# Kernel optimization log

Hardware: AMD Instinct MI355X
Metric: run time of the kernel (lower is better)

Reference implementation:

```python
import jax, jax.numpy as jnp
import numpy as np

D = 1024          # d_model
H = 16            # num_attention_heads
HD = D // H       # head_dim
WIN = 512         # attention_window (total)
W = WIN // 2      # one-sided window
S = 4096          # seq_len
B = 2             # batch
NEG = jnp.finfo(jnp.float32).min


def setup_inputs() -> dict:
    key = jax.random.key(0)
    ks = jax.random.split(key, 9)
    sc = 0.02
    return {
        "query": jax.random.normal(ks[0], (S, B, D), dtype=jnp.float32),
        "Wq": jax.random.normal(ks[1], (D, D), dtype=jnp.float32) * sc,
        "bq": jnp.zeros((D,), dtype=jnp.float32),
        "Wk": jax.random.normal(ks[2], (D, D), dtype=jnp.float32) * sc,
        "bk": jnp.zeros((D,), dtype=jnp.float32),
        "Wv": jax.random.normal(ks[3], (D, D), dtype=jnp.float32) * sc,
        "bv": jnp.zeros((D,), dtype=jnp.float32),
        "Wo": jax.random.normal(ks[4], (D, D), dtype=jnp.float32) * sc,
        "bo": jnp.zeros((D,), dtype=jnp.float32),
    }


def _heads(x):  # [B,S,D] -> [B,H,S,HD]
    b, s, _ = x.shape
    return x.reshape(b, s, H, HD).transpose(0, 2, 1, 3)


def reference(query, Wq, bq, Wk, bk, Wv, bv, Wo, bo):
    s, b, d = query.shape
    x = query.transpose(1, 0, 2)                       # [B,S,D]
    q = _heads(x @ Wq + bq) / jnp.sqrt(jnp.float32(HD))  # [B,H,S,HD]
    k = _heads(x @ Wk + bk)
    v = _heads(x @ Wv + bv)

    nc = s // W                                        # number of chunks
    # pad keys/values with one window of zeros on each side of seq axis
    kp = jnp.pad(k, ((0, 0), (0, 0), (W, W), (0, 0)))  # [B,H,S+2W,HD]
    vp = jnp.pad(v, ((0, 0), (0, 0), (W, W), (0, 0)))
    idx = jnp.arange(nc)[:, None] * W + jnp.arange(3 * W)[None, :]  # [nc,3W]
    kc = kp[:, :, idx]                                 # [B,H,nc,3W,HD]
    vc = vp[:, :, idx]
    qc = q.reshape(b, H, nc, W, HD)                    # [B,H,nc,W,HD]

    scores = jnp.einsum("bhcrd,bhckd->bhcrk", qc, kc)  # [B,H,nc,W,3W]

    r = jnp.arange(W)[:, None]                         # query offset in chunk
    kk = jnp.arange(3 * W)[None, :]
    band = (kk >= r) & (kk <= r + 2 * W)               # |kpos-qpos| <= W
    kpos = jnp.arange(nc)[:, None, None] * W + kk[None] - W   # [nc,1,3W] global key pos
    mask = band[None] & (kpos >= 0) & (kpos < s)       # [nc,W,3W]

    scores = jnp.where(mask[None, None], scores, NEG)
    probs = jax.nn.softmax(scores, axis=-1)
    out = jnp.einsum("bhcrk,bhckd->bhcrd", probs, vc)  # [B,H,nc,W,HD]
    out = out.reshape(b, H, s, HD).transpose(0, 2, 1, 3).reshape(b, s, d)
    out = out.transpose(1, 0, 2)                       # [S,B,D]
    return out @ Wo + bo
```

## Files before the change

kernel.cpp:

```cpp
#include <hip/hip_runtime.h>
#include <hip/hip_bf16.h>

#define SEQ 4096
#define BATCH 2
#define DMODEL 1024
#define NH 16
#define HDIM 64
#define NEGM (-1.0e30f)
#define NT 16

typedef __attribute__((ext_vector_type(8))) short bf16x8;
typedef __attribute__((ext_vector_type(8))) unsigned short us8;
typedef __attribute__((ext_vector_type(4))) unsigned short us4;
typedef __attribute__((ext_vector_type(4))) float f32x4;

__device__ __forceinline__ unsigned short f2bf(float f) {
    union { float f; unsigned u; } v; v.f = f;
    unsigned u = v.u;
    return (unsigned short)((u + 0x7fffu + ((u >> 16) & 1u)) >> 16);
}

#define GL16(g, l)                                                              \
    __builtin_amdgcn_global_load_lds(                                           \
        (const __attribute__((address_space(1))) unsigned int*)(g),             \
        (__attribute__((address_space(3))) unsigned int*)(l), 16, 0, 0)

__global__ __launch_bounds__(256) void prep_all(const float* __restrict__ Wq,
                                                const float* __restrict__ Wk,
                                                const float* __restrict__ Wv,
                                                const float* __restrict__ Wo,
                                                const float* __restrict__ query,
                                                const float* __restrict__ bq,
                                                const float* __restrict__ bk,
                                                const float* __restrict__ bv,
                                                unsigned short* __restrict__ wcat,
                                                unsigned short* __restrict__ wot,
                                                unsigned short* __restrict__ xb,
                                                float* __restrict__ bcat) {
    __shared__ float tile[64][65];
    const int bid = blockIdx.x;
    const int tid = threadIdx.x;
    if (bid < 1024) {
        const int z = bid >> 8, by = (bid >> 4) & 15, bx = bid & 15;
        const float* W = (z == 0) ? Wq : (z == 1) ? Wk : (z == 2) ? Wv : Wo;
        unsigned short* Wt = (z == 3) ? wot : wcat + (size_t)z * 1024 * 1024;
        const float scale = (z == 0) ? 0.125f : 1.0f;
        const int n0 = bx * 64, k0 = by * 64;
        const int tx = tid & 63, ty = tid >> 6;
        for (int dy = ty; dy < 64; dy += 4)
            tile[dy][tx] = W[(size_t)(k0 + dy) * DMODEL + n0 + tx];
        __syncthreads();
        for (int dy = ty; dy < 64; dy += 4)
            Wt[(size_t)(n0 + dy) * DMODEL + k0 + tx] = f2bf(tile[tx][dy] * scale);
    } else if (bid < 9216) {
        int t = (bid - 1024) * 256 + tid;
        int d4 = (t & 255) * 4;
        int row = t >> 8;
        int b = row >> 12, s = row & (SEQ - 1);
        float4 v = *(const float4*)(query + ((size_t)s * BATCH + b) * DMODEL + d4);
        us4 o;
        o[0] = f2bf(v.x); o[1] = f2bf(v.y); o[2] = f2bf(v.z); o[3] = f2bf(v.w);
        *(us4*)(xb + (size_t)row * DMODEL + d4) = o;
    } else {
        int i = (bid - 9216) * 256 + tid;
        float v;
        if (i < 1024) v = bq[i] * 0.125f;
        else if (i < 2048) v = bk[i - 1024];
        else v = bv[i - 2048];
        bcat[i] = v;
    }
}

__device__ __forceinline__ void store_qkv(float v0, float v1, float v2, float v3,
                                          int row0, int col, float bval,
                                          unsigned short* __restrict__ qb,
                                          unsigned short* __restrict__ kb,
                                          unsigned short* __restrict__ vtb) {
    const int proj = col >> 10;
    const int ch = col & 1023;
    const int h = ch >> 6, hd = ch & 63;
    float vv[4] = {v0, v1, v2, v3};
    if (proj == 2) {
        const int b = row0 >> 12, s = row0 & (SEQ - 1);
        us4 o;
#pragma unroll
        for (int r = 0; r < 4; ++r) o[r] = f2bf(vv[r] + bval);
        *(us4*)(vtb + ((size_t)(b * NH + h) * HDIM + hd) * SEQ + s) = o;
    } else {
        unsigned short* dst = (proj == 0) ? qb : kb;
#pragma unroll
        for (int r = 0; r < 4; ++r) {
            const int row = row0 + r;
            const int b = row >> 12, s = row & (SEQ - 1);
            dst[((size_t)(b * NH + h) * SEQ + s) * HDIM + hd] = f2bf(vv[r] + bval);
        }
    }
}

__global__ __launch_bounds__(512) void gemm192(const unsigned short* __restrict__ A,
                                               const unsigned short* __restrict__ Bt,
                                               const float* __restrict__ bias,
                                               unsigned short* __restrict__ qb,
                                               unsigned short* __restrict__ kb,
                                               unsigned short* __restrict__ vtb) {
    __shared__ __align__(16) unsigned short lds[57344];
    const int tid = threadIdx.x;
    const int lane = tid & 63, wid = tid >> 6;
    const int lr = lane & 15, lg = lane >> 4;
    const int wm = wid >> 1, wn = wid & 1;
    const int cpx = (int)gridDim.x >> 3;
    const int orig = ((int)blockIdx.x & 7) * cpx + ((int)blockIdx.x >> 3);
    const int m0 = (orig >> 4) * 256;
    const int n0 = (orig & 15) * 192;

    const int srow = wid * 8 + (lane >> 3);
    const int scol = ((lane & 7) ^ (lane >> 3)) << 3;

    f32x4 acc[4][6];
#pragma unroll
    for (int m = 0; m < 4; ++m)
#pragma unroll
        for (int n = 0; n < 6; ++n) {
            f32x4 z = {0.f, 0.f, 0.f, 0.f};
            acc[m][n] = z;
        }

    const unsigned short* gA = A + (size_t)(m0 + srow) * DMODEL + scol;
    const unsigned short* gB = Bt + (size_t)(n0 + srow) * DMODEL + scol;

#define STAGE192(kt, bsel)                                                       \
    do {                                                                         \
        const unsigned short* ga_ = gA + (kt) * 64;                              \
        unsigned short* la_ = &lds[(bsel) * 28672 + wid * 512];                  \
        _Pragma("unroll")                                                        \
        for (int r_ = 0; r_ < 4; ++r_)                                           \
            GL16(ga_ + (size_t)r_ * 64 * DMODEL, la_ + r_ * 4096);               \
        const unsigned short* gb_ = gB + (kt) * 64;                              \
        unsigned short* lb_ = &lds[(bsel) * 28672 + 16384 + wid * 512];          \
        _Pragma("unroll")                                                        \
        for (int r_ = 0; r_ < 3; ++r_)                                           \
            GL16(gb_ + (size_t)r_ * 64 * DMODEL, lb_ + r_ * 4096);               \
    } while (0)

    STAGE192(0, 0);
    asm volatile("s_waitcnt vmcnt(0)" ::: "memory");
    __builtin_amdgcn_s_barrier();
    asm volatile("" ::: "memory");

    const int swz = (lr & 7) << 3;
    for (int t = 0; t < NT; ++t) {
        if (t + 1 < NT) STAGE192(t + 1, (t + 1) & 1);
        const unsigned short* Ab = &lds[(t & 1) * 28672];
        const unsigned short* Bb = Ab + 16384;
#pragma unroll
        for (int ks = 0; ks < 2; ++ks) {
            const int kc = (ks * 32 + lg * 8) ^ swz;
            bf16x8 af[4], bfr[6];
#pragma unroll
            for (int fm = 0; fm < 4; ++fm)
                af[fm] = *(const bf16x8*)&Ab[(wm * 64 + fm * 16 + lr) * 64 + kc];
#pragma unroll
            for (int fn = 0; fn < 6; ++fn)
                bfr[fn] = *(const bf16x8*)&Bb[(wn * 96 + fn * 16 + lr) * 64 + kc];
            __builtin_amdgcn_s_setprio(1);
#pragma unroll
            for (int fm = 0; fm < 4; ++fm)
#pragma unroll
                for (int fn = 0; fn < 6; ++fn)
                    acc[fm][fn] = __builtin_amdgcn_mfma_f32_16x16x32_bf16(af[fm], bfr[fn], acc[fm][fn], 0, 0, 0);
            __builtin_amdgcn_s_setprio(0);
        }
        __builtin_amdgcn_sched_barrier(0);
        asm volatile("s_waitcnt lgkmcnt(0)" ::: "memory");
        asm volatile("s_waitcnt vmcnt(0)" ::: "memory");
        __builtin_amdgcn_s_barrier();
        asm volatile("" ::: "memory");
    }
#undef STAGE192

#pragma unroll
    for (int fn = 0; fn < 6; ++fn) {
        const int col = n0 + wn * 96 + fn * 16 + lr;
        const float bval = bias[col];
#pragma unroll
        for (int fm = 0; fm < 4; ++fm) {
            const int row0 = m0 + wm * 64 + fm * 16 + lg * 4;
            store_qkv(acc[fm][fn][0], acc[fm][fn][1], acc[fm][fn][2], acc[fm][fn][3],
                      row0, col, bval, qb, kb, vtb);
        }
    }
}

__global__ __launch_bounds__(256, 4) void gemm128o(const unsigned short* __restrict__ A,
                                                   const unsigned short* __restrict__ Bt,
                                                   const float* __restrict__ bias,
                                                   float* __restrict__ out) {
    __shared__ __align__(16) unsigned short lds[16384];
    const int tid = threadIdx.x;
    const int lane = tid & 63, wid = tid >> 6;
    const int lr = lane & 15, lg = lane >> 4;
    const int wm = wid >> 1, wn = wid & 1;
    const int cpx = (int)gridDim.x >> 3;
    const int orig = ((int)blockIdx.x & 7) * cpx + ((int)blockIdx.x >> 3);
    const int m0 = (orig >> 3) * 128;
    const int n0 = (orig & 7) * 128;

    const int srow = wid * 8 + (lane >> 3);
    const int scol = ((lane & 7) ^ (lane >> 3)) << 3;

    f32x4 acc[4][4];
#pragma unroll
    for (int m = 0; m < 4; ++m)
#pragma unroll
        for (int n = 0; n < 4; ++n) {
            f32x4 z = {0.f, 0.f, 0.f, 0.f};
            acc[m][n] = z;
        }

    const unsigned short* gA = A + (size_t)(m0 + srow) * DMODEL + scol;
    const unsigned short* gB = Bt + (size_t)(n0 + srow) * DMODEL + scol;
    const int swz = (lr & 7) << 3;

    for (int t = 0; t < NT; ++t) {
        {
            const unsigned short* ga_ = gA + t * 64;
            unsigned short* la_ = &lds[wid * 512];
#pragma unroll
            for (int r_ = 0; r_ < 4; ++r_)
                GL16(ga_ + (size_t)r_ * 32 * DMODEL, la_ + r_ * 2048);
            const unsigned short* gb_ = gB + t * 64;
            unsigned short* lb_ = &lds[8192 + wid * 512];
#pragma unroll
            for (int r_ = 0; r_ < 4; ++r_)
                GL16(gb_ + (size_t)r_ * 32 * DMODEL, lb_ + r_ * 2048);
        }
        asm volatile("s_waitcnt vmcnt(0)" ::: "memory");
        __builtin_amdgcn_s_barrier();
        asm volatile("" ::: "memory");
#pragma unroll
        for (int ks = 0; ks < 2; ++ks) {
            const int kc = (ks * 32 + lg * 8) ^ swz;
            bf16x8 af[4], bfr[4];
#pragma unroll
            for (int fm = 0; fm < 4; ++fm)
                af[fm] = *(const bf16x8*)&lds[(wm * 64 + fm * 16 + lr) * 64 + kc];
#pragma unroll
            for (int fn = 0; fn < 4; ++fn)
                bfr[fn] = *(const bf16x8*)&lds[8192 + (wn * 64 + fn * 16 + lr) * 64 + kc];
            __builtin_amdgcn_s_setprio(1);
#pragma unroll
            for (int fm = 0; fm < 4; ++fm)
#pragma unroll
                for (int fn = 0; fn < 4; ++fn)
                    acc[fm][fn] = __builtin_amdgcn_mfma_f32_16x16x32_bf16(af[fm], bfr[fn], acc[fm][fn], 0, 0, 0);
            __builtin_amdgcn_s_setprio(0);
        }
        __builtin_amdgcn_sched_barrier(0);
        asm volatile("s_waitcnt lgkmcnt(0)" ::: "memory");
        __builtin_amdgcn_s_barrier();
        asm volatile("" ::: "memory");
    }

#pragma unroll
    for (int fn = 0; fn < 4; ++fn) {
        const int col = n0 + wn * 64 + fn * 16 + lr;
        const float bval = bias[col];
#pragma unroll
        for (int fm = 0; fm < 4; ++fm) {
            const int row0 = m0 + wm * 64 + fm * 16 + lg * 4;
#pragma unroll
            for (int r = 0; r < 4; ++r) {
                const int row = row0 + r;
                const int b = row >> 12, s = row & (SEQ - 1);
                out[((size_t)s * BATCH + b) * DMODEL + col] = acc[fm][fn][r] + bval;
            }
        }
    }
}

__global__ __launch_bounds__(512) void attn_kernel(const unsigned short* __restrict__ qb,
                                                   const unsigned short* __restrict__ kb,
                                                   const unsigned short* __restrict__ vtb,
                                                   unsigned short* __restrict__ ao) {
    __shared__ __align__(16) unsigned short Ks[64][72];
    __shared__ __align__(16) unsigned short Vs[64][72];
    __shared__ __align__(16) unsigned short Ps[8][16][72];
    const int tid = threadIdx.x;
    const int lane = tid & 63, wid = tid >> 6;
    const int lr = lane & 15, lg = lane >> 4;
    const int blk = ((int)blockIdx.x & 7) * 128 + ((int)blockIdx.x >> 3);
    const int qc = blk & 31, h = (blk >> 5) & 15, b = blk >> 9;
    const int q0 = qc * 128;
    const unsigned short* Qh = qb + (size_t)(b * NH + h) * SEQ * HDIM;
    const unsigned short* Kh = kb + (size_t)(b * NH + h) * SEQ * HDIM;
    const unsigned short* Vh = vtb + (size_t)(b * NH + h) * HDIM * SEQ;
    const int qw = q0 + wid * 16;

    bf16x8 qf0 = *(const bf16x8*)(Qh + (size_t)(qw + lr) * HDIM + lg * 8);
    bf16x8 qf1 = *(const bf16x8*)(Qh + (size_t)(qw + lr) * HDIM + 32 + lg * 8);

    f32x4 oacc[4];
    float lsum[4];
#pragma unroll
    for (int n = 0; n < 4; ++n) {
        f32x4 z = {0.f, 0.f, 0.f, 0.f};
        oacc[n] = z;
    }
#pragma unroll
    for (int r = 0; r < 4; ++r) lsum[r] = 0.f;

    int lo = q0 - 256; if (lo < 0) lo = 0;
    int hi = q0 + 384; if (hi > SEQ) hi = SEQ;

    const int srow = tid >> 3, sseg = (tid & 7) * 8;

    us8 kpre = *(const us8*)(Kh + (size_t)(lo + srow) * HDIM + sseg);
    us8 vpre = *(const us8*)(Vh + (size_t)srow * SEQ + lo + sseg);

    for (int kt = lo; kt < hi; kt += 64) {
        __syncthreads();
        *(us8*)&Ks[srow][sseg] = kpre;
        *(us8*)&Vs[srow][sseg] = vpre;
        if (kt + 64 < hi) {
            kpre = *(const us8*)(Kh + (size_t)(kt + 64 + srow) * HDIM + sseg);
            vpre = *(const us8*)(Vh + (size_t)srow * SEQ + kt + 64 + sseg);
        }
        __builtin_amdgcn_sched_barrier(0);
        __syncthreads();

        f32x4 sf[4];
        __builtin_amdgcn_s_setprio(1);
#pragma unroll
        for (int n = 0; n < 4; ++n) {
            bf16x8 kf0 = *(const bf16x8*)&Ks[n * 16 + lr][lg * 8];
            bf16x8 kf1 = *(const bf16x8*)&Ks[n * 16 + lr][32 + lg * 8];
            f32x4 z = {0.f, 0.f, 0.f, 0.f};
            sf[n] = __builtin_amdgcn_mfma_f32_16x16x32_bf16(qf0, kf0, z, 0, 0, 0);
            sf[n] = __builtin_amdgcn_mfma_f32_16x16x32_bf16(qf1, kf1, sf[n], 0, 0, 0);
        }
        __builtin_amdgcn_s_setprio(0);
        const bool full = (kt >= qw - 241) && (kt + 63 <= qw + 256);
        if (!full) {
#pragma unroll
            for (int r = 0; r < 4; ++r) {
                const int qpos = qw + lg * 4 + r;
#pragma unroll
                for (int n = 0; n < 4; ++n) {
                    const int kpos = kt + n * 16 + lr;
                    if (kpos < qpos - 256 || kpos > qpos + 256) sf[n][r] = NEGM;
                }
            }
        }
#pragma unroll
        for (int n = 0; n < 4; ++n)
#pragma unroll
            for (int r = 0; r < 4; ++r) {
                const float p = __expf(sf[n][r]);
                lsum[r] += p;
                Ps[wid][lg * 4 + r][n * 16 + lr] = f2bf(p);
            }

        asm volatile("s_waitcnt lgkmcnt(0)" ::: "memory");
        __builtin_amdgcn_s_setprio(1);
#pragma unroll
        for (int ks = 0; ks < 2; ++ks) {
            bf16x8 pf = *(const bf16x8*)&Ps[wid][lr][ks * 32 + lg * 8];
#pragma unroll
            for (int n = 0; n < 4; ++n) {
                bf16x8 vf = *(const bf16x8*)&Vs[n * 16 + lr][ks * 32 + lg * 8];
                oacc[n] = __builtin_amdgcn_mfma_f32_16x16x32_bf16(pf, vf, oacc[n], 0, 0, 0);
            }
        }
        __builtin_amdgcn_s_setprio(0);
    }

#pragma unroll
    for (int d = 1; d < 16; d <<= 1)
#pragma unroll
        for (int r = 0; r < 4; ++r) lsum[r] += __shfl_xor(lsum[r], d, 64);

#pragma unroll
    for (int n = 0; n < 4; ++n)
#pragma unroll
        for (int r = 0; r < 4; ++r) {
            const int row = qw + lg * 4 + r;
            const float o = oacc[n][r] / lsum[r];
            ao[((size_t)b * SEQ + row) * DMODEL + h * HDIM + n * 16 + lr] = f2bf(o);
        }
}

extern "C" void kernel_launch(void* const* d_in, const int* in_sizes, int n_in,
                              void* d_out, int out_size, void* d_ws, size_t ws_size,
                              hipStream_t stream) {
    (void)in_sizes; (void)n_in; (void)out_size; (void)ws_size;
    const float* query = (const float*)d_in[0];
    const float* Wq = (const float*)d_in[1];
    const float* bq = (const float*)d_in[2];
    const float* Wk = (const float*)d_in[3];
    const float* bk = (const float*)d_in[4];
    const float* Wv = (const float*)d_in[5];
    const float* bv = (const float*)d_in[6];
    const float* Wo = (const float*)d_in[7];
    const float* bo = (const float*)d_in[8];
    float* out = (float*)d_out;

    char* ws = (char*)d_ws;
    unsigned short* xb   = (unsigned short*)ws;
    unsigned short* wcat = (unsigned short*)(ws + (16ull << 20));
    unsigned short* wot  = (unsigned short*)(ws + (22ull << 20));
    float*          bcat = (float*)(ws + (24ull << 20));
    unsigned short* qb   = (unsigned short*)(ws + (25ull << 20));
    unsigned short* kb   = (unsigned short*)(ws + (41ull << 20));
    unsigned short* vtb  = (unsigned short*)(ws + (57ull << 20));
    unsigned short* ao   = xb;

    prep_all<<<9228, 256, 0, stream>>>(Wq, Wk, Wv, Wo, query, bq, bk, bv,
                                       wcat, wot, xb, bcat);
    gemm192<<<512, 512, 0, stream>>>(xb, wcat, bcat, qb, kb, vtb);
    attn_kernel<<<1024, 512, 0, stream>>>(qb, kb, vtb, ao);
    gemm128o<<<512, 256, 0, stream>>>(ao, wot, bo, out);
}
```

Measured before the change: 140.5 us.

## Keep attention probabilities in registers via transposed QK^T and lane shuffles

The QK^T MFMA is computed transposed (K as A operand), so each lane holds scores for a single query row. The probabilities are packed to bf16 and redistributed with cross-lane shuffles to form the A operand of the PV MFMA directly, which removes the per-wave LDS staging buffer, its stores, the waitcnt and the reloads. The row-sum reduction is simplified accordingly, and launch bounds now request higher occupancy. The exchange costs extra shuffles and selects and interleaves the softmax work with the MFMAs per 32-key slice.

```diff
diff --git a/kernel.cpp b/kernel.cpp
--- a/kernel.cpp
+++ b/kernel.cpp
@@ -18,6 +18,10 @@
     union { float f; unsigned u; } v; v.f = f;
     unsigned u = v.u;
     return (unsigned short)((u + 0x7fffu + ((u >> 16) & 1u)) >> 16);
+}
+
+__device__ __forceinline__ unsigned packbf(float a, float b) {
+    return (unsigned)f2bf(a) | ((unsigned)f2bf(b) << 16);
 }
 
 #define GL16(g, l)                                                              \
@@ -278,13 +282,12 @@
     }
 }
 
-__global__ __launch_bounds__(512) void attn_kernel(const unsigned short* __restrict__ qb,
-                                                   const unsigned short* __restrict__ kb,
-                                                   const unsigned short* __restrict__ vtb,
-                                                   unsigned short* __restrict__ ao) {
+__global__ __launch_bounds__(512, 8) void attn_kernel(const unsigned short* __restrict__ qb,
+                                                      const unsigned short* __restrict__ kb,
+                                                      const unsigned short* __restrict__ vtb,
+                                                      unsigned short* __restrict__ ao) {
     __shared__ __align__(16) unsigned short Ks[64][72];
     __shared__ __align__(16) unsigned short Vs[64][72];
-    __shared__ __align__(16) unsigned short Ps[8][16][72];
     const int tid = threadIdx.x;
     const int lane = tid & 63, wid = tid >> 6;
     const int lr = lane & 15, lg = lane >> 4;
@@ -295,19 +298,19 @@
     const unsigned short* Kh = kb + (size_t)(b * NH + h) * SEQ * HDIM;
     const unsigned short* Vh = vtb + (size_t)(b * NH + h) * HDIM * SEQ;
     const int qw = q0 + wid * 16;
+    const int qpos = qw + lr;
+    const int odd = lg & 1;
 
     bf16x8 qf0 = *(const bf16x8*)(Qh + (size_t)(qw + lr) * HDIM + lg * 8);
     bf16x8 qf1 = *(const bf16x8*)(Qh + (size_t)(qw + lr) * HDIM + 32 + lg * 8);
 
     f32x4 oacc[4];
-    float lsum[4];
+    float lsum = 0.f;
 #pragma unroll
     for (int n = 0; n < 4; ++n) {
         f32x4 z = {0.f, 0.f, 0.f, 0.f};
         oacc[n] = z;
     }
-#pragma unroll
-    for (int r = 0; r < 4; ++r) lsum[r] = 0.f;
 
     int lo = q0 - 256; if (lo < 0) lo = 0;
     int hi = q0 + 384; if (hi > SEQ) hi = SEQ;
@@ -328,63 +331,67 @@
         __builtin_amdgcn_sched_barrier(0);
         __syncthreads();
 
-        f32x4 sf[4];
-        __builtin_amdgcn_s_setprio(1);
-#pragma unroll
-        for (int n = 0; n < 4; ++n) {
-            bf16x8 kf0 = *(const bf16x8*)&Ks[n * 16 + lr][lg * 8];
-            bf16x8 kf1 = *(const bf16x8*)&Ks[n * 16 + lr][32 + lg * 8];
-            f32x4 z = {0.f, 0.f, 0.f, 0.f};
-            sf[n] = __builtin_amdgcn_mfma_f32_16x16x32_bf16(qf0, kf0, z, 0, 0, 0);
-            sf[n] = __builtin_amdgcn_mfma_f32_16x16x32_bf16(qf1, kf1, sf[n], 0, 0, 0);
-        }
-        __builtin_amdgcn_s_setprio(0);
         const bool full = (kt >= qw - 241) && (kt + 63 <= qw + 256);
-        if (!full) {
-#pragma unroll
-            for (int r = 0; r < 4; ++r) {
-                const int qpos = qw + lg * 4 + r;
-#pragma unroll
-                for (int n = 0; n < 4; ++n) {
-                    const int kpos = kt + n * 16 + lr;
-                    if (kpos < qpos - 256 || kpos > qpos + 256) sf[n][r] = NEGM;
+#pragma unroll
+        for (int ks = 0; ks < 2; ++ks) {
+            unsigned gdw[2][4];
+#pragma unroll
+            for (int bi = 0; bi < 2; ++bi) {
+                const int n = ks * 2 + bi;
+                bf16x8 kf0 = *(const bf16x8*)&Ks[n * 16 + lr][lg * 8];
+                bf16x8 kf1 = *(const bf16x8*)&Ks[n * 16 + lr][32 + lg * 8];
+                f32x4 z = {0.f, 0.f, 0.f, 0.f};
+                __builtin_amdgcn_s_setprio(1);
+                f32x4 sf = __builtin_amdgcn_mfma_f32_16x16x32_bf16(kf0, qf0, z, 0, 0, 0);
+                sf = __builtin_amdgcn_mfma_f32_16x16x32_bf16(kf1, qf1, sf, 0, 0, 0);
+                __builtin_amdgcn_s_setprio(0);
+                if (!full) {
+#pragma unroll
+                    for (int r = 0; r < 4; ++r) {
+                        const int kpos = kt + n * 16 + lg * 4 + r;
+                        if (kpos < qpos - 256 || kpos > qpos + 256) sf[r] = NEGM;
+                    }
                 }
+                const float p0 = __expf(sf[0]);
+                const float p1 = __expf(sf[1]);
+                const float p2 = __expf(sf[2]);
+                const float p3 = __expf(sf[3]);
+                lsum += (p0 + p1) + (p2 + p3);
+                const unsigned dA = packbf(p0, p1);
+                const unsigned dB = packbf(p2, p3);
+                const unsigned rA = __shfl_xor((int)dA, 16, 64);
+                const unsigned rB = __shfl_xor((int)dB, 16, 64);
+                gdw[bi][0] = odd ? rA : dA;
+                gdw[bi][1] = odd ? rB : dB;
+                gdw[bi][2] = odd ? dA : rA;
+                gdw[bi][3] = odd ? dB : rB;
             }
-        }
-#pragma unroll
-        for (int n = 0; n < 4; ++n)
-#pragma unroll
-            for (int r = 0; r < 4; ++r) {
-                const float p = __expf(sf[n][r]);
-                lsum[r] += p;
-                Ps[wid][lg * 4 + r][n * 16 + lr] = f2bf(p);
+            union { unsigned u[4]; bf16x8 v; } pu;
+#pragma unroll
+            for (int j = 0; j < 4; ++j) pu.u[j] = odd ? gdw[1][j] : gdw[0][j];
+            const int koff = (ks * 2 + odd) * 16 + (lg >> 1) * 8;
+            __builtin_amdgcn_s_setprio(1);
+#pragma unroll
+            for (int n = 0; n < 4; ++n) {
+                bf16x8 vf = *(const bf16x8*)&Vs[n * 16 + lr][koff];
+                oacc[n] = __builtin_amdgcn_mfma_f32_16x16x32_bf16(pu.v, vf, oacc[n], 0, 0, 0);
             }
-
-        asm volatile("s_waitcnt lgkmcnt(0)" ::: "memory");
-        __builtin_amdgcn_s_setprio(1);
-#pragma unroll
-        for (int ks = 0; ks < 2; ++ks) {
-            bf16x8 pf = *(const bf16x8*)&Ps[wid][lr][ks * 32 + lg * 8];
-#pragma unroll
-            for (int n = 0; n < 4; ++n) {
-                bf16x8 vf = *(const bf16x8*)&Vs[n * 16 + lr][ks * 32 + lg * 8];
-                oacc[n] = __builtin_amdgcn_mfma_f32_16x16x32_bf16(pf, vf, oacc[n], 0, 0, 0);
-            }
-        }
-        __builtin_amdgcn_s_setprio(0);
-    }
-
-#pragma unroll
-    for (int d = 1; d < 16; d <<= 1)
-#pragma unroll
-        for (int r = 0; r < 4; ++r) lsum[r] += __shfl_xor(lsum[r], d, 64);
+            __builtin_amdgcn_s_setprio(0);
+        }
+    }
+
+    lsum += __shfl_xor(lsum, 16, 64);
+    lsum += __shfl_xor(lsum, 32, 64);
+    float ls[4];
+#pragma unroll
+    for (int r = 0; r < 4; ++r) ls[r] = __shfl(lsum, lg * 4 + r, 64);
 
 #pragma unroll
     for (int n = 0; n < 4; ++n)
 #pragma unroll
         for (int r = 0; r < 4; ++r) {
             const int row = qw + lg * 4 + r;
-            const float o = oacc[n][r] / lsum[r];
+            const float o = oacc[n][r] / ls[r];
             ao[((size_t)b * SEQ + row) * DMODEL + h * HDIM + n * 16 + lr] = f2bf(o);
         }
 }
```

Result: slower. 178.9 us (+27.3%).
